# Performance work log

Hardware: AMD Instinct MI355X
Metric: run time of the kernel (lower is better)

## Reference

```python
import jax, jax.numpy as jnp
import numpy as np

BN_EPS = 1e-5

# Binary_a: sign forward, hard-tanh STE backward (grad zeroed where |x| >= 1)
@jax.custom_vjp
def binary_act(x):
    return jnp.sign(x)

def _ba_fwd(x):
    return jnp.sign(x), x

def _ba_bwd(x, g):
    return (jnp.where((x > -1.0) & (x < 1.0), g, 0.0),)

binary_act.defvjp(_ba_fwd, _ba_bwd)

# Binary_w: sign forward, identity STE backward
@jax.custom_vjp
def binary_w(x):
    return jnp.sign(x)

def _bw_fwd(x):
    return jnp.sign(x), None

def _bw_bwd(_, g):
    return (g,)

binary_w.defvjp(_bw_fwd, _bw_bwd)


def setup_inputs() -> dict:
    key = jax.random.key(0)
    k1, k2, k3 = jax.random.split(key, 3)
    B, Cin, Cout, H, Wd, K = 32, 256, 256, 56, 56, 3
    x = jax.random.normal(k1, (B, Cin, H, Wd), dtype=jnp.float32)
    weight = jax.random.normal(k2, (Cout, Cin, K, K), dtype=jnp.float32) * 0.05
    bias = jax.random.normal(k3, (Cout,), dtype=jnp.float32) * 0.01
    gamma = jnp.ones((Cout,), dtype=jnp.float32)
    beta = jnp.zeros((Cout,), dtype=jnp.float32)
    return {"x": x, "weight": weight, "bias": bias, "gamma": gamma, "beta": beta}


def reference(x, weight, bias, gamma, beta):
    # activation binarization (A=2)
    xb = binary_act(x)
    # weight quantization (W=2): mean-center over in-channel dim, clamp to [-1,1]
    # (done on .data in torch -> values change but no grad through this step)
    wc_val = jnp.clip(weight - jnp.mean(weight, axis=1, keepdims=True), -1.0, 1.0)
    wc = weight + jax.lax.stop_gradient(wc_val - weight)
    # per-output-filter scale alpha = E[|w|] over (in, kh, kw)
    alpha = jnp.mean(jnp.abs(wc), axis=(1, 2, 3), keepdims=True)
    wq = binary_w(wc) * alpha  # [O,I,K,K]
    # conv2d, stride 1, padding 1, groups 1
    y = jax.lax.conv_general_dilated(
        xb, wq, window_strides=(1, 1), padding=((1, 1), (1, 1)),
        dimension_numbers=("NCHW", "OIHW", "NCHW"))
    y = y + bias[None, :, None, None]
    # BatchNorm2d, training-mode forward (biased batch stats)
    mean = jnp.mean(y, axis=(0, 2, 3), keepdims=True)
    var = jnp.mean(jnp.square(y - mean), axis=(0, 2, 3), keepdims=True)
    y = (y - mean) * jax.lax.rsqrt(var + BN_EPS)
    y = y * gamma[None, :, None, None] + beta[None, :, None, None]
    # last_relu=1
    return jax.nn.relu(y)
```

## Files before the change

kernel.cpp:

```cpp
#include <hip/hip_runtime.h>
#include <stdint.h>

typedef unsigned long long u64;
typedef unsigned int u32;
typedef int v4i __attribute__((ext_vector_type(4)));
typedef int v16i __attribute__((ext_vector_type(16)));
typedef short s4v __attribute__((ext_vector_type(4)));
typedef short s8v __attribute__((ext_vector_type(8)));
typedef float f4v __attribute__((ext_vector_type(4)));
typedef u32 u32x4 __attribute__((ext_vector_type(4)));

#define B_    32
#define CIN   256
#define COUT  256
#define H_    56
#define W_    56
#define HW    3136
#define NPOS  100352
#define HBLK  28
#define NPACKBLK 784


__global__ __launch_bounds__(256) void k_prep(
    const float* __restrict__ x,
    const float* __restrict__ wgt,
    u32* __restrict__ xbits,
    int8_t* __restrict__ Bfrag,
    float* __restrict__ alpha,
    int* __restrict__ ssum,
    unsigned long long* __restrict__ qsum)
{
    const int tid = threadIdx.x;

    if (blockIdx.x < NPACKBLK) {
        const int j2 = blockIdx.x / 98;
        const int p4 = (blockIdx.x - j2 * 98) * 256 + tid;
        const int pos0 = p4 * 4;
        const int b = pos0 / HW;
        const int hw = pos0 - b * HW;
        const float* xp = x + (size_t)b * CIN * HW + (size_t)j2 * 32 * HW + hw;
        u32 b0 = 0, b1 = 0, b2 = 0, b3 = 0;
#pragma unroll 16
        for (int k = 0; k < 32; ++k) {
            const float4 v = *(const float4*)(xp + (size_t)k * HW);
            b0 |= (u32)(v.x > 0.0f) << k;
            b1 |= (u32)(v.y > 0.0f) << k;
            b2 |= (u32)(v.z > 0.0f) << k;
            b3 |= (u32)(v.w > 0.0f) << k;
        }
        u32* xp4 = xbits + (size_t)j2 * NPOS + pos0;
        *(u32x4*)xp4 = u32x4{b0, b1, b2, b3};
        return;
    }

    const int o = blockIdx.x - NPACKBLK;
    const int i = tid;
    const int wave = i >> 6, lane = i & 63;
    __shared__ float sred[4][12];

    if (i == 0) { ssum[o] = 0; qsum[o] = 0ULL; }

    float w9[9];
#pragma unroll
    for (int t = 0; t < 9; ++t) w9[t] = wgt[(o * 256 + i) * 9 + t];

    float m[9];
#pragma unroll
    for (int t = 0; t < 9; ++t) m[t] = w9[t];
#pragma unroll
    for (int s = 1; s < 64; s <<= 1)
#pragma unroll
        for (int t = 0; t < 9; ++t) m[t] += __shfl_xor(m[t], s, 64);
    if (lane == 0) {
#pragma unroll
        for (int t = 0; t < 9; ++t) sred[wave][t] = m[t];
    }
    __syncthreads();
#pragma unroll
    for (int t = 0; t < 9; ++t)
        m[t] = (sred[0][t] + sred[1][t] + sred[2][t] + sred[3][t]) * (1.0f / 256.0f);

    float wc[9];
    float asum = 0.0f;
#pragma unroll
    for (int t = 0; t < 9; ++t) {
        float v = w9[t] - m[t];
        v = fminf(fmaxf(v, -1.0f), 1.0f);
        wc[t] = v;
        asum += fabsf(v);
    }
#pragma unroll
    for (int s = 1; s < 64; s <<= 1) asum += __shfl_xor(asum, s, 64);
    __syncthreads();
    if (lane == 0) sred[wave][9] = asum;
    __syncthreads();
    if (i == 0)
        alpha[o] = (sred[0][9] + sred[1][9] + sred[2][9] + sred[3][9]) * (1.0f / 2304.0f);

#pragma unroll
    for (int t = 0; t < 9; ++t) {
        const int8_t sv = (wc[t] > 0.0f) ? (int8_t)1 : (int8_t)-1;
        const int kk = t * 8 + (i >> 5);
        const size_t addr =
            ((((size_t)(o >> 6) * 72 + kk) * 2 + ((o >> 5) & 1)) * 64
             + (size_t)(((i >> 4) & 1) * 32 + (o & 31))) * 16 + (i & 15);
        Bfrag[addr] = sv;
    }
}

#define MFMA_I8(acc, a, b) \
    asm volatile("v_mfma_i32_32x32x32_i8 %0, %1, %2, %0" : "+a"(acc) : "v"(a), "v"(b))

__global__ __launch_bounds__(256, 2) void kc_mfma(
    const u32* __restrict__ xbits,
    const int8_t* __restrict__ Bfrag,
    short* __restrict__ S,
    int* __restrict__ ssum,
    unsigned long long* __restrict__ qsum)
{
    const int blk = blockIdx.x;
    const int b = blk / HBLK;
    const int h0 = (blk - b * HBLK) * 2;
    const int tid = threadIdx.x;

    __shared__ u32 ldsb[4 * 58 * 64];

    for (int it = tid; it < 4 * 58 * 16; it += 256) {
        const int r = it / 928;
        const int rem = it - r * 928;
        const int wp = rem >> 4;
        const int g = rem & 15;
        const int hr = h0 - 1 + r;
        const int w_in = wp - 1;
        const bool inb = (hr >= 0) && (hr < H_) && (w_in >= 0) && (w_in < W_);
        u32 chunk16 = 0;
        if (inb) {
            const u32 word = xbits[(size_t)(g >> 1) * NPOS
                                   + (size_t)(b * HW + hr * W_ + w_in)];
            chunk16 = (word >> ((g & 1) * 16)) & 0xFFFFu;
        }
        u32 out4[4];
#pragma unroll
        for (int d = 0; d < 4; ++d) {
            const u32 nib = (chunk16 >> (4 * d)) & 0xFu;
            const u32 m1 = (nib * 0x00204081u) & 0x01010101u;
            const u32 inv = m1 ^ 0x01010101u;
            out4[d] = inb ? (0x01010101u ^ (inv * 0xFEu)) : 0u;
        }
        const int gs = (g ^ wp) & 15;
        u32* dst = &ldsb[((r * 58 + wp) << 6) + gs * 4];
        dst[0] = out4[0]; dst[1] = out4[1]; dst[2] = out4[2]; dst[3] = out4[3];
    }
    __syncthreads();

    const int m0 = tid & 31;
    const int lh = (tid >> 5) & 1;
    const int wv = tid >> 6;
    const int8_t* smem = (const int8_t*)ldsb;
    const int8_t* Bp = Bfrag + (size_t)wv * 147456 + (size_t)(tid & 63) * 16;

    auto ldA = [&](int kk, int mt) -> v4i {
        const int tap = kk >> 3, s = kk & 7;
        const int dh = tap / 3;
        const int dw = tap - dh * 3;
        const int r = (mt >> 1) + dh;
        const int wpm = (mt & 1) ? min(32 + m0 + dw, 57) : (m0 + dw);
        const int P = ((r * 58 + wpm) << 8) + ((((wpm & 15) ^ lh)) << 4);
        return *(const v4i*)(smem + (P ^ (s << 5)));
    };
    auto ldB = [&](int kk, int ntl) -> v4i {
        return *(const v4i*)(Bp + (size_t)kk * 2048 + ntl * 1024);
    };

    v16i acc[4][2] = {};
    v4i A[4][2], Bb[2][2];

#pragma unroll
    for (int mt = 0; mt < 4; ++mt) A[mt][0] = ldA(0, mt);
    Bb[0][0] = ldB(0, 0);
    Bb[1][0] = ldB(0, 1);

#pragma unroll
    for (int kk = 0; kk < 72; ++kk) {
        const int cur = kk & 1, nxt = cur ^ 1;
        if (kk < 71) {
#pragma unroll
            for (int mt = 0; mt < 4; ++mt) A[mt][nxt] = ldA(kk + 1, mt);
            Bb[0][nxt] = ldB(kk + 1, 0);
            Bb[1][nxt] = ldB(kk + 1, 1);
        }
        __builtin_amdgcn_s_setprio(1);
#pragma unroll
        for (int mt = 0; mt < 4; ++mt) {
            MFMA_I8(acc[mt][0], A[mt][cur], Bb[0][cur]);
            MFMA_I8(acc[mt][1], A[mt][cur], Bb[1][cur]);
        }
        __builtin_amdgcn_s_setprio(0);
    }

    asm volatile("s_nop 7\n\ts_nop 7\n\ts_nop 7"
                 : "+a"(acc[0][0]), "+a"(acc[0][1]), "+a"(acc[1][0]), "+a"(acc[1][1]),
                   "+a"(acc[2][0]), "+a"(acc[2][1]), "+a"(acc[3][0]), "+a"(acc[3][1]));

    const int n0 = wv * 64 + m0;
    int s0 = 0, s1 = 0, q0 = 0, q1 = 0;

    __syncthreads();
    short* eP = (short*)ldsb;

#pragma unroll
    for (int mt = 0; mt < 4; ++mt) {
        const int posb = (mt >> 1) * 56 + ((mt & 1) << 5) + (lh << 2);
        const int nq = (mt & 1) ? 3 : 4;
#pragma unroll
        for (int q = 0; q < nq; ++q) {
            s4v pk0, pk1;
#pragma unroll
            for (int j = 0; j < 4; ++j) {
                const int v0 = acc[mt][0][4 * q + j];
                const int v1 = acc[mt][1][4 * q + j];
                s0 += v0; q0 += v0 * v0; s1 += v1; q1 += v1 * v1;
                pk0[j] = (short)v0;
                pk1[j] = (short)v1;
            }
            const int pq = posb + 8 * q;
            *(s4v*)((char*)eP + n0 * 232 + pq * 2) = pk0;
            *(s4v*)((char*)eP + (n0 + 32) * 232 + pq * 2) = pk1;
        }
    }
    __syncthreads();

    {
        const int l = tid & 63;
        if (l < 56) {
            const int ch2 = l / 14;
            const int ii = l - ch2 * 14;
            const size_t posb2 = (size_t)b * HW + (size_t)h0 * W_;
#pragma unroll
            for (int t2 = 0; t2 < 16; ++t2) {
                const int cg = wv * 64 + t2 * 4 + ch2;
                const v4i val = *(const v4i*)((const char*)eP + cg * 232 + ii * 16);
                *(v4i*)(S + (size_t)cg * NPOS + posb2 + ii * 8) = val;
            }
        }
    }

    s0 += __shfl_xor(s0, 32, 64); q0 += __shfl_xor(q0, 32, 64);
    s1 += __shfl_xor(s1, 32, 64); q1 += __shfl_xor(q1, 32, 64);
    if (lh == 0) {
        atomicAdd(&ssum[n0], s0);
        atomicAdd(&qsum[n0], (unsigned long long)(long long)q0);
        atomicAdd(&ssum[n0 + 32], s1);
        atomicAdd(&qsum[n0 + 32], (unsigned long long)(long long)q1);
    }
}

__global__ __launch_bounds__(256) void kb_apply(
    const short* __restrict__ S,
    const int* __restrict__ ssum,
    const unsigned long long* __restrict__ qsum,
    const float* __restrict__ alpha,
    const float* __restrict__ gamma,
    const float* __restrict__ beta,
    float* __restrict__ out)
{
    const int blk = blockIdx.x;
    const int c = blk >> 5;
    const int b = blk & 31;

    const double N = (double)NPOS;
    const double meanS = (double)ssum[c] / N;
    const double varS = (double)qsum[c] / N - meanS * meanS;
    const double a = (double)alpha[c];
    const double rstd = 1.0 / sqrt(a * a * varS + 1e-5);
    const double g = (double)gamma[c];
    const float scale = (float)(g * a * rstd);
    const float shift = (float)((double)beta[c] - g * a * meanS * rstd);

    const s8v* src = (const s8v*)(S + (size_t)c * NPOS + (size_t)b * HW);
    float* dst = out + ((size_t)(b * COUT + c)) * HW;

    for (int idx = threadIdx.x; idx < HW / 8; idx += 256) {
        const s8v v = src[idx];
        f4v o0, o1;
#pragma unroll
        for (int j = 0; j < 4; ++j)
            o0[j] = fmaxf(fmaf((float)v[j], scale, shift), 0.0f);
#pragma unroll
        for (int j = 0; j < 4; ++j)
            o1[j] = fmaxf(fmaf((float)v[4 + j], scale, shift), 0.0f);
        *(f4v*)(dst + idx * 8) = o0;
        *(f4v*)(dst + idx * 8 + 4) = o1;
    }
}

extern "C" void kernel_launch(void* const* d_in, const int* in_sizes, int n_in,
                              void* d_out, int out_size, void* d_ws, size_t ws_size,
                              hipStream_t stream) {
    const float* x     = (const float*)d_in[0];
    const float* wgt   = (const float*)d_in[1];
    const float* gamma = (const float*)d_in[3];
    const float* beta  = (const float*)d_in[4];
    float* out = (float*)d_out;

    char* ws = (char*)d_ws;
    int8_t* Bfrag = (int8_t*)(ws + 0);
    float* alpha = (float*)(ws + 589824);
    int*   ssum  = (int*)(ws + 590848);
    unsigned long long* qsum = (unsigned long long*)(ws + 591872);
    u32*   xbits = (u32*)(ws + 593920);
    short* Sarr  = (short*)(ws + 3805184);

    k_prep<<<NPACKBLK + 256, 256, 0, stream>>>(x, wgt, xbits, Bfrag, alpha, ssum, qsum);
    kc_mfma<<<B_ * HBLK, 256, 0, stream>>>(xbits, Bfrag, Sarr, ssum, qsum);
    kb_apply<<<COUT * B_, 256, 0, stream>>>(Sarr, ssum, qsum, alpha, gamma, beta, out);
}
```

Measured before the change: 275.5 us.

## Split conv MFMA block across 8 waves with half the M-tiles each

Doubles the conv kernel's block to 512 threads. Each wave now handles one output row (rowsel) and a 64-channel slice, with 2 M-tiles instead of 4. This halves per-wave accumulator and A-register use and raises wave-level parallelism, so memory and LDS latency can be hidden better. The cost is that each B fragment is loaded by two waves, which doubles B traffic per block, and occupancy is now bound by the 512-thread block size and LDS.

```diff
diff --git a/kernel.cpp b/kernel.cpp
--- a/kernel.cpp
+++ b/kernel.cpp
@@ -111,7 +111,7 @@
 #define MFMA_I8(acc, a, b) \
     asm volatile("v_mfma_i32_32x32x32_i8 %0, %1, %2, %0" : "+a"(acc) : "v"(a), "v"(b))
 
-__global__ __launch_bounds__(256, 2) void kc_mfma(
+__global__ __launch_bounds__(512, 4) void kc_mfma(
     const u32* __restrict__ xbits,
     const int8_t* __restrict__ Bfrag,
     short* __restrict__ S,
@@ -125,7 +125,7 @@
 
     __shared__ u32 ldsb[4 * 58 * 64];
 
-    for (int it = tid; it < 4 * 58 * 16; it += 256) {
+    for (int it = tid; it < 4 * 58 * 16; it += 512) {
         const int r = it / 928;
         const int rem = it - r * 928;
         const int wp = rem >> 4;
@@ -156,15 +156,17 @@
     const int m0 = tid & 31;
     const int lh = (tid >> 5) & 1;
     const int wv = tid >> 6;
+    const int nsl = wv & 3;
+    const int rowsel = wv >> 2;
     const int8_t* smem = (const int8_t*)ldsb;
-    const int8_t* Bp = Bfrag + (size_t)wv * 147456 + (size_t)(tid & 63) * 16;
+    const int8_t* Bp = Bfrag + (size_t)nsl * 147456 + (size_t)(tid & 63) * 16;
 
     auto ldA = [&](int kk, int mt) -> v4i {
         const int tap = kk >> 3, s = kk & 7;
         const int dh = tap / 3;
         const int dw = tap - dh * 3;
-        const int r = (mt >> 1) + dh;
-        const int wpm = (mt & 1) ? min(32 + m0 + dw, 57) : (m0 + dw);
+        const int r = rowsel + dh;
+        const int wpm = mt ? min(32 + m0 + dw, 57) : (m0 + dw);
         const int P = ((r * 58 + wpm) << 8) + ((((wpm & 15) ^ lh)) << 4);
         return *(const v4i*)(smem + (P ^ (s << 5)));
     };
@@ -172,46 +174,41 @@
         return *(const v4i*)(Bp + (size_t)kk * 2048 + ntl * 1024);
     };
 
-    v16i acc[4][2] = {};
-    v4i A[4][2], Bb[2][2];
-
-#pragma unroll
-    for (int mt = 0; mt < 4; ++mt) A[mt][0] = ldA(0, mt);
-    Bb[0][0] = ldB(0, 0);
-    Bb[1][0] = ldB(0, 1);
+    v16i acc[2][2] = {};
+    v4i A[2][2], Bb[2][2];
+
+    A[0][0] = ldA(0, 0); A[1][0] = ldA(0, 1);
+    Bb[0][0] = ldB(0, 0); Bb[1][0] = ldB(0, 1);
 
 #pragma unroll
     for (int kk = 0; kk < 72; ++kk) {
         const int cur = kk & 1, nxt = cur ^ 1;
         if (kk < 71) {
-#pragma unroll
-            for (int mt = 0; mt < 4; ++mt) A[mt][nxt] = ldA(kk + 1, mt);
+            A[0][nxt] = ldA(kk + 1, 0); A[1][nxt] = ldA(kk + 1, 1);
             Bb[0][nxt] = ldB(kk + 1, 0);
             Bb[1][nxt] = ldB(kk + 1, 1);
         }
         __builtin_amdgcn_s_setprio(1);
-#pragma unroll
-        for (int mt = 0; mt < 4; ++mt) {
-            MFMA_I8(acc[mt][0], A[mt][cur], Bb[0][cur]);
-            MFMA_I8(acc[mt][1], A[mt][cur], Bb[1][cur]);
-        }
+        MFMA_I8(acc[0][0], A[0][cur], Bb[0][cur]);
+        MFMA_I8(acc[0][1], A[0][cur], Bb[1][cur]);
+        MFMA_I8(acc[1][0], A[1][cur], Bb[0][cur]);
+        MFMA_I8(acc[1][1], A[1][cur], Bb[1][cur]);
         __builtin_amdgcn_s_setprio(0);
     }
 
     asm volatile("s_nop 7\n\ts_nop 7\n\ts_nop 7"
-                 : "+a"(acc[0][0]), "+a"(acc[0][1]), "+a"(acc[1][0]), "+a"(acc[1][1]),
-                   "+a"(acc[2][0]), "+a"(acc[2][1]), "+a"(acc[3][0]), "+a"(acc[3][1]));
-
-    const int n0 = wv * 64 + m0;
+                 : "+a"(acc[0][0]), "+a"(acc[0][1]), "+a"(acc[1][0]), "+a"(acc[1][1]));
+
+    const int n0 = nsl * 64 + m0;
     int s0 = 0, s1 = 0, q0 = 0, q1 = 0;
 
     __syncthreads();
     short* eP = (short*)ldsb;
 
 #pragma unroll
-    for (int mt = 0; mt < 4; ++mt) {
-        const int posb = (mt >> 1) * 56 + ((mt & 1) << 5) + (lh << 2);
-        const int nq = (mt & 1) ? 3 : 4;
+    for (int mt = 0; mt < 2; ++mt) {
+        const int posb = rowsel * 56 + (mt << 5) + (lh << 2);
+        const int nq = mt ? 3 : 4;
 #pragma unroll
         for (int q = 0; q < nq; ++q) {
             s4v pk0, pk1;
@@ -232,13 +229,14 @@
 
     {
         const int l = tid & 63;
+        const int grp = tid >> 6;
         if (l < 56) {
             const int ch2 = l / 14;
             const int ii = l - ch2 * 14;
             const size_t posb2 = (size_t)b * HW + (size_t)h0 * W_;
 #pragma unroll
-            for (int t2 = 0; t2 < 16; ++t2) {
-                const int cg = wv * 64 + t2 * 4 + ch2;
+            for (int t2 = 0; t2 < 8; ++t2) {
+                const int cg = grp * 32 + t2 * 4 + ch2;
                 const v4i val = *(const v4i*)((const char*)eP + cg * 232 + ii * 16);
                 *(v4i*)(S + (size_t)cg * NPOS + posb2 + ii * 8) = val;
             }
@@ -312,6 +310,6 @@
     short* Sarr  = (short*)(ws + 3805184);
 
     k_prep<<<NPACKBLK + 256, 256, 0, stream>>>(x, wgt, xbits, Bfrag, alpha, ssum, qsum);
-    kc_mfma<<<B_ * HBLK, 256, 0, stream>>>(xbits, Bfrag, Sarr, ssum, qsum);
+    kc_mfma<<<B_ * HBLK, 512, 0, stream>>>(xbits, Bfrag, Sarr, ssum, qsum);
     kb_apply<<<COUT * B_, 256, 0, stream>>>(Sarr, ssum, qsum, alpha, gamma, beta, out);
 }
```

Result: slower. 288.9 us (+4.9%).

## Fuse prep, conv and BN-apply into one cooperative persistent kernel

Applied to the files above, without the earlier changes.

Replaces the three kernel launches with a single cooperative kernel of 512 blocks. The phases are separated by grid syncs, and conv tiles are handed out dynamically through an atomic counter. The aim is to cut launch gaps and tail effects between phases, in exchange for grid-sync overhead and a fixed 512-block occupancy in the pack and apply phases. The old kernels remain as a fallback if the cooperative launch fails. The tile counter is reset by block 0 at kernel start, which depends on that reset landing before any block reads the counter after the first grid sync.

```diff
diff --git a/kernel.cpp b/kernel.cpp
--- a/kernel.cpp
+++ b/kernel.cpp
@@ -1,5 +1,8 @@
 #include <hip/hip_runtime.h>
+#include <hip/hip_cooperative_groups.h>
 #include <stdint.h>
+
+namespace cg = cooperative_groups;
 
 typedef unsigned long long u64;
 typedef unsigned int u32;
@@ -18,45 +21,43 @@
 #define HW    3136
 #define NPOS  100352
 #define HBLK  28
+#define NTILE 896
 #define NPACKBLK 784
-
-
-__global__ __launch_bounds__(256) void k_prep(
-    const float* __restrict__ x,
-    const float* __restrict__ wgt,
-    u32* __restrict__ xbits,
-    int8_t* __restrict__ Bfrag,
-    float* __restrict__ alpha,
-    int* __restrict__ ssum,
-    unsigned long long* __restrict__ qsum)
-{
-    const int tid = threadIdx.x;
-
-    if (blockIdx.x < NPACKBLK) {
-        const int j2 = blockIdx.x / 98;
-        const int p4 = (blockIdx.x - j2 * 98) * 256 + tid;
-        const int pos0 = p4 * 4;
-        const int b = pos0 / HW;
-        const int hw = pos0 - b * HW;
-        const float* xp = x + (size_t)b * CIN * HW + (size_t)j2 * 32 * HW + hw;
-        u32 b0 = 0, b1 = 0, b2 = 0, b3 = 0;
+#define NGRID 512
+
+__device__ int g_tile_cnt;
+
+
+
+__device__ __forceinline__ void phase_pack(
+    int task, int tid, const float* __restrict__ x, u32* __restrict__ xbits)
+{
+    const int j2 = task / 98;
+    const int p4 = (task - j2 * 98) * 256 + tid;
+    const int pos0 = p4 * 4;
+    const int b = pos0 / HW;
+    const int hw = pos0 - b * HW;
+    const float* xp = x + (size_t)b * CIN * HW + (size_t)j2 * 32 * HW + hw;
+    u32 b0 = 0, b1 = 0, b2 = 0, b3 = 0;
 #pragma unroll 16
-        for (int k = 0; k < 32; ++k) {
-            const float4 v = *(const float4*)(xp + (size_t)k * HW);
-            b0 |= (u32)(v.x > 0.0f) << k;
-            b1 |= (u32)(v.y > 0.0f) << k;
-            b2 |= (u32)(v.z > 0.0f) << k;
-            b3 |= (u32)(v.w > 0.0f) << k;
-        }
-        u32* xp4 = xbits + (size_t)j2 * NPOS + pos0;
-        *(u32x4*)xp4 = u32x4{b0, b1, b2, b3};
-        return;
-    }
-
-    const int o = blockIdx.x - NPACKBLK;
+    for (int k = 0; k < 32; ++k) {
+        const float4 v = *(const float4*)(xp + (size_t)k * HW);
+        b0 |= (u32)(v.x > 0.0f) << k;
+        b1 |= (u32)(v.y > 0.0f) << k;
+        b2 |= (u32)(v.z > 0.0f) << k;
+        b3 |= (u32)(v.w > 0.0f) << k;
+    }
+    u32* xp4 = xbits + (size_t)j2 * NPOS + pos0;
+    *(u32x4*)xp4 = u32x4{b0, b1, b2, b3};
+}
+
+__device__ __forceinline__ void phase_wprep(
+    int o, int tid, const float* __restrict__ wgt, int8_t* __restrict__ Bfrag,
+    float* __restrict__ alpha, int* __restrict__ ssum,
+    unsigned long long* __restrict__ qsum, float (*sred)[12])
+{
     const int i = tid;
     const int wave = i >> 6, lane = i & 63;
-    __shared__ float sred[4][12];
 
     if (i == 0) { ssum[o] = 0; qsum[o] = 0ULL; }
 
@@ -111,19 +112,13 @@
 #define MFMA_I8(acc, a, b) \
     asm volatile("v_mfma_i32_32x32x32_i8 %0, %1, %2, %0" : "+a"(acc) : "v"(a), "v"(b))
 
-__global__ __launch_bounds__(256, 2) void kc_mfma(
-    const u32* __restrict__ xbits,
-    const int8_t* __restrict__ Bfrag,
-    short* __restrict__ S,
-    int* __restrict__ ssum,
-    unsigned long long* __restrict__ qsum)
-{
-    const int blk = blockIdx.x;
+__device__ __forceinline__ void phase_conv(
+    int blk, int tid, const u32* __restrict__ xbits, const int8_t* __restrict__ Bfrag,
+    short* __restrict__ S, int* __restrict__ ssum,
+    unsigned long long* __restrict__ qsum, u32* ldsb)
+{
     const int b = blk / HBLK;
     const int h0 = (blk - b * HBLK) * 2;
-    const int tid = threadIdx.x;
-
-    __shared__ u32 ldsb[4 * 58 * 64];
 
     for (int it = tid; it < 4 * 58 * 16; it += 256) {
         const int r = it / 928;
@@ -255,18 +250,14 @@
     }
 }
 
-__global__ __launch_bounds__(256) void kb_apply(
-    const short* __restrict__ S,
-    const int* __restrict__ ssum,
-    const unsigned long long* __restrict__ qsum,
-    const float* __restrict__ alpha,
-    const float* __restrict__ gamma,
-    const float* __restrict__ beta,
+__device__ __forceinline__ void phase_apply(
+    int task, int tid, const short* __restrict__ S, const int* __restrict__ ssum,
+    const unsigned long long* __restrict__ qsum, const float* __restrict__ alpha,
+    const float* __restrict__ gamma, const float* __restrict__ beta,
     float* __restrict__ out)
 {
-    const int blk = blockIdx.x;
-    const int c = blk >> 5;
-    const int b = blk & 31;
+    const int c = task >> 5;
+    const int b = task & 31;
 
     const double N = (double)NPOS;
     const double meanS = (double)ssum[c] / N;
@@ -280,7 +271,7 @@
     const s8v* src = (const s8v*)(S + (size_t)c * NPOS + (size_t)b * HW);
     float* dst = out + ((size_t)(b * COUT + c)) * HW;
 
-    for (int idx = threadIdx.x; idx < HW / 8; idx += 256) {
+    for (int idx = tid; idx < HW / 8; idx += 256) {
         const s8v v = src[idx];
         f4v o0, o1;
 #pragma unroll
@@ -292,6 +283,75 @@
         *(f4v*)(dst + idx * 8) = o0;
         *(f4v*)(dst + idx * 8 + 4) = o1;
     }
+}
+
+__global__ __launch_bounds__(256, 2) void k_fused(
+    const float* __restrict__ x, const float* __restrict__ wgt,
+    const float* __restrict__ gamma, const float* __restrict__ beta,
+    float* __restrict__ out,
+    u32* __restrict__ xbits, int8_t* __restrict__ Bfrag, float* __restrict__ alpha,
+    int* __restrict__ ssum, unsigned long long* __restrict__ qsum,
+    short* __restrict__ S)
+{
+    __shared__ u32 ldsb[4 * 58 * 64];
+    __shared__ float sred[4][12];
+    __shared__ int sh_t;
+
+    const int blk = blockIdx.x;
+    const int tid = threadIdx.x;
+
+    if (blk == 0 && tid == 0) g_tile_cnt = 0;
+
+    for (int task = blk; task < NPACKBLK + 256; task += NGRID) {
+        if (task < NPACKBLK) phase_pack(task, tid, x, xbits);
+        else phase_wprep(task - NPACKBLK, tid, wgt, Bfrag, alpha, ssum, qsum, sred);
+    }
+
+    __threadfence();
+    cg::this_grid().sync();
+
+    for (;;) {
+        if (tid == 0) sh_t = atomicAdd(&g_tile_cnt, 1);
+        __syncthreads();
+        const int t = sh_t;
+        if (t >= NTILE) break;
+        phase_conv(t, tid, xbits, Bfrag, S, ssum, qsum, ldsb);
+        __syncthreads();
+    }
+
+    __threadfence();
+    cg::this_grid().sync();
+
+    for (int task = blk; task < COUT * B_; task += NGRID)
+        phase_apply(task, tid, S, ssum, qsum, alpha, gamma, beta, out);
+}
+
+__global__ __launch_bounds__(256) void k_prep(
+    const float* __restrict__ x, const float* __restrict__ wgt,
+    u32* __restrict__ xbits, int8_t* __restrict__ Bfrag, float* __restrict__ alpha,
+    int* __restrict__ ssum, unsigned long long* __restrict__ qsum)
+{
+    __shared__ float sred[4][12];
+    if (blockIdx.x < NPACKBLK) phase_pack(blockIdx.x, threadIdx.x, x, xbits);
+    else phase_wprep(blockIdx.x - NPACKBLK, threadIdx.x, wgt, Bfrag, alpha, ssum, qsum, sred);
+}
+
+__global__ __launch_bounds__(256, 2) void kc_mfma(
+    const u32* __restrict__ xbits, const int8_t* __restrict__ Bfrag,
+    short* __restrict__ S, int* __restrict__ ssum,
+    unsigned long long* __restrict__ qsum)
+{
+    __shared__ u32 ldsb[4 * 58 * 64];
+    phase_conv(blockIdx.x, threadIdx.x, xbits, Bfrag, S, ssum, qsum, ldsb);
+}
+
+__global__ __launch_bounds__(256) void kb_apply(
+    const short* __restrict__ S, const int* __restrict__ ssum,
+    const unsigned long long* __restrict__ qsum, const float* __restrict__ alpha,
+    const float* __restrict__ gamma, const float* __restrict__ beta,
+    float* __restrict__ out)
+{
+    phase_apply(blockIdx.x, threadIdx.x, S, ssum, qsum, alpha, gamma, beta, out);
 }
 
 extern "C" void kernel_launch(void* const* d_in, const int* in_sizes, int n_in,
@@ -311,7 +371,14 @@
     u32*   xbits = (u32*)(ws + 593920);
     short* Sarr  = (short*)(ws + 3805184);
 
-    k_prep<<<NPACKBLK + 256, 256, 0, stream>>>(x, wgt, xbits, Bfrag, alpha, ssum, qsum);
-    kc_mfma<<<B_ * HBLK, 256, 0, stream>>>(xbits, Bfrag, Sarr, ssum, qsum);
-    kb_apply<<<COUT * B_, 256, 0, stream>>>(Sarr, ssum, qsum, alpha, gamma, beta, out);
-}
+    void* args[] = {(void*)&x, (void*)&wgt, (void*)&gamma, (void*)&beta, (void*)&out,
+                    (void*)&xbits, (void*)&Bfrag, (void*)&alpha,
+                    (void*)&ssum, (void*)&qsum, (void*)&Sarr};
+    hipError_t e = hipLaunchCooperativeKernel((const void*)k_fused, dim3(NGRID),
+                                              dim3(256), args, 0, stream);
+    if (e != hipSuccess) {
+        k_prep<<<NPACKBLK + 256, 256, 0, stream>>>(x, wgt, xbits, Bfrag, alpha, ssum, qsum);
+        kc_mfma<<<NTILE, 256, 0, stream>>>(xbits, Bfrag, Sarr, ssum, qsum);
+        kb_apply<<<COUT * B_, 256, 0, stream>>>(Sarr, ssum, qsum, alpha, gamma, beta, out);
+    }
+}
```

After: 788.1 us. +186.1%, slower.
